# Kernel optimization log

Measured on AMD Instinct MI355X. Metric: run time of the kernel, lower is better.

## Reference

```python
import jax, jax.numpy as jnp
import numpy as np

EMBED_DIM = 1024
NUM_HEADS = 16
HEAD_DIM = EMBED_DIM // NUM_HEADS


def setup_inputs() -> dict:
    key = jax.random.key(0)
    ks = jax.random.split(key, 10)
    s = 1.0 / np.sqrt(EMBED_DIM)
    x = jax.random.normal(ks[0], (2, 2048, EMBED_DIM), dtype=jnp.float32)
    Wq = jax.random.uniform(ks[1], (EMBED_DIM, EMBED_DIM), jnp.float32, -s, s)
    bq = jax.random.uniform(ks[2], (EMBED_DIM,), jnp.float32, -s, s)
    Wk = jax.random.uniform(ks[3], (EMBED_DIM, EMBED_DIM), jnp.float32, -s, s)
    bk = jax.random.uniform(ks[4], (EMBED_DIM,), jnp.float32, -s, s)
    Wv = jax.random.uniform(ks[5], (EMBED_DIM, EMBED_DIM), jnp.float32, -s, s)
    bv = jax.random.uniform(ks[6], (EMBED_DIM,), jnp.float32, -s, s)
    Wo = jax.random.uniform(ks[7], (EMBED_DIM, EMBED_DIM), jnp.float32, -s, s)
    bo = jax.random.uniform(ks[8], (EMBED_DIM,), jnp.float32, -s, s)
    return {"x": x, "Wq": Wq, "bq": bq, "Wk": Wk, "bk": bk,
            "Wv": Wv, "bv": bv, "Wo": Wo, "bo": bo}


def reference(x, Wq, bq, Wk, bk, Wv, bv, Wo, bo):
    b, s, e = x.shape
    h, d = NUM_HEADS, HEAD_DIM
    scale = d ** -0.5
    # projections (torch Linear: x @ W.T + b; here W stored as [in, out])
    q = (x @ Wq + bq).reshape(b, s, h, d)
    k = (x @ Wk + bk).reshape(b, s, h, d)
    v = (x @ Wv + bv).reshape(b, s, h, d)
    logits = jnp.einsum('bqhd,bkhd->bhqk', q, k) * scale
    causal = jnp.tril(jnp.ones((s, s), dtype=bool))  # keep lower triangle
    logits = jnp.where(causal, logits, -jnp.inf)
    attn = jax.nn.softmax(logits, axis=-1)
    out = jnp.einsum('bhqk,bkhd->bqhd', attn, v).reshape(b, s, e)
    return out @ Wo + bo
```

## Files before the change

kernel.cpp:

```cpp
#include <hip/hip_runtime.h>


#define EMB 1024
#define SEQ 2048
#define NB 2
#define NH 16
#define HD 64

#define QSCALE 0.18033688011112042f

typedef float f32x4 __attribute__((ext_vector_type(4)));
typedef float floatx4 __attribute__((ext_vector_type(4)));
typedef short short8 __attribute__((ext_vector_type(8)));
typedef __bf16 bf16x8 __attribute__((ext_vector_type(8)));
typedef __bf16 bf16x2 __attribute__((ext_vector_type(2)));
typedef unsigned short ushortx4 __attribute__((ext_vector_type(4)));
typedef unsigned int uintx4 __attribute__((ext_vector_type(4)));

__device__ __forceinline__ unsigned short bf16u(float f) {
  __bf16 h = (__bf16)f;
  return __builtin_bit_cast(unsigned short, h);
}

__device__ __forceinline__ unsigned pkbf(float lo, float hi) {
  bf16x2 v;
  v[0] = (__bf16)lo;
  v[1] = (__bf16)hi;
  return __builtin_bit_cast(unsigned, v);
}

__device__ __forceinline__ f32x4 mfma16(short8 a, short8 b, f32x4 c) {
  return __builtin_amdgcn_mfma_f32_16x16x32_bf16(
      __builtin_bit_cast(bf16x8, a), __builtin_bit_cast(bf16x8, b), c, 0, 0, 0);
}

__device__ __forceinline__ void gload16(const void* g, void* lds) {
  __builtin_amdgcn_global_load_lds(
      (const __attribute__((address_space(1))) unsigned int*)g,
      (__attribute__((address_space(3))) unsigned int*)lds, 16, 0, 0);
}

__global__ __launch_bounds__(256) void cvt_x_kernel(
    const float* __restrict__ x, unsigned short* __restrict__ out) {
  const int idx = (blockIdx.x * 256 + threadIdx.x) * 4;
  floatx4 v = *(const floatx4*)(x + idx);
  ushortx4 o;
  #pragma unroll
  for (int i = 0; i < 4; ++i) o[i] = bf16u(v[i]);
  *(ushortx4*)(out + idx) = o;
}

__global__ __launch_bounds__(256) void cvt_w4_kernel(
    const float* __restrict__ W0, const float* __restrict__ W1,
    const float* __restrict__ W2, const float* __restrict__ W3,
    unsigned short* __restrict__ T0, unsigned short* __restrict__ T1,
    unsigned short* __restrict__ T2, unsigned short* __restrict__ T3) {
  __shared__ unsigned short tile[32][33];
  const int z = blockIdx.z;
  const float* W = (z == 0) ? W0 : (z == 1) ? W1 : (z == 2) ? W2 : W3;
  unsigned short* WT = (z == 0) ? T0 : (z == 1) ? T1 : (z == 2) ? T2 : T3;
  const int k0 = blockIdx.x * 32, n0 = blockIdx.y * 32;
  const int t = threadIdx.x;
  const int r = t >> 3, c = (t & 7) * 4;
  floatx4 v = *(const floatx4*)(W + (k0 + r) * EMB + n0 + c);
  #pragma unroll
  for (int i = 0; i < 4; ++i) tile[r][c + i] = bf16u(v[i]);
  __syncthreads();
  ushortx4 o;
  #pragma unroll
  for (int i = 0; i < 4; ++i) o[i] = tile[c + i][r];
  *(ushortx4*)(WT + (n0 + r) * EMB + k0 + c) = o;
}

#define GEMM_KLOOP(OP1, OP2)                                                 \
    for (int kk = 0; kk < 64; kk += 32) {                                    \
      short8 a[4], b[4];                                                     \
      _Pragma("unroll")                                                      \
      for (int i = 0; i < 4; ++i)                                            \
        a[i] = *(const short8*)(As + (wr * 64 + i * 16 + ln) * 64 + kk + g * 8); \
      _Pragma("unroll")                                                      \
      for (int j = 0; j < 4; ++j)                                            \
        b[j] = *(const short8*)(Bs + (wc * 64 + j * 16 + ln) * 64 + kk + g * 8); \
      _Pragma("unroll")                                                      \
      for (int i = 0; i < 4; ++i)                                            \
        _Pragma("unroll")                                                    \
        for (int j = 0; j < 4; ++j)                                          \
          acc[i][j] = mfma16(OP1, OP2, acc[i][j]);                           \
    }

__global__ __launch_bounds__(256) void gemm_qkv_kernel(
    const unsigned short* __restrict__ Xb,
    const unsigned short* __restrict__ W0, const unsigned short* __restrict__ W1,
    const unsigned short* __restrict__ W2,
    const float* __restrict__ b0, const float* __restrict__ b1,
    const float* __restrict__ b2,
    unsigned short* __restrict__ Qo, unsigned short* __restrict__ Ko,
    unsigned short* __restrict__ Vo) {
  __shared__ __align__(16) unsigned short As[128 * 64];
  __shared__ __align__(16) unsigned short Bs[128 * 64];
  const int z = blockIdx.z;
  const unsigned short* Wt = (z == 0) ? W0 : ((z == 1) ? W1 : W2);
  const float* bias = (z == 0) ? b0 : ((z == 1) ? b1 : b2);
  const bool sw = (z != 2);
  const int m0 = blockIdx.y * 128, n0 = blockIdx.x * 128;
  const int tid = threadIdx.x, l = tid & 63, w = tid >> 6;
  const int g = l >> 4, ln = l & 15;
  const int wr = w >> 1, wc = w & 1;

  f32x4 acc[4][4];
  #pragma unroll
  for (int i = 0; i < 4; ++i)
    #pragma unroll
    for (int j = 0; j < 4; ++j) acc[i][j] = (f32x4){0.f, 0.f, 0.f, 0.f};

  for (int kt = 0; kt < 16; ++kt) {
    const int kb = kt * 64;
    #pragma unroll
    for (int it = 0; it < 4; ++it) {
      const int chunk = w * 4 + it;
      const int lin = chunk * 64 + l;
      const int row = lin >> 3, col = (lin & 7) * 8;
      gload16(Xb + (m0 + row) * EMB + kb + col, (char*)As + chunk * 1024);
      gload16(Wt + (n0 + row) * EMB + kb + col, (char*)Bs + chunk * 1024);
    }
    __syncthreads();
    if (sw) {
      GEMM_KLOOP(b[j], a[i])
    } else {
      GEMM_KLOOP(a[i], b[j])
    }
    __syncthreads();
  }

  const int mb = m0 + wr * 64, nb = n0 + wc * 64;
  if (sw) {
    unsigned short* dst = (z == 0) ? Qo : Ko;
    const float osc = (z == 0) ? QSCALE : 1.0f;
    #pragma unroll
    for (int j = 0; j < 4; ++j) {
      const int n = nb + j * 16 + 4 * g;
      floatx4 bv_ = *(const floatx4*)(bias + n);
      const int h = n >> 6, d = n & 63;
      #pragma unroll
      for (int i = 0; i < 4; ++i) {
        const int m = mb + i * 16 + ln;
        const int bb = m >> 11, ss = m & 2047;
        ushortx4 o;
        #pragma unroll
        for (int e = 0; e < 4; ++e) o[e] = bf16u((acc[i][j][e] + bv_[e]) * osc);
        *(ushortx4*)(dst + ((bb * NH + h) * SEQ + ss) * HD + d) = o;
      }
    }
  } else {
    #pragma unroll
    for (int j = 0; j < 4; ++j) {
      const int n = nb + j * 16 + ln;
      const float bgain = bias[n];
      const int h = n >> 6, d = n & 63;
      #pragma unroll
      for (int i = 0; i < 4; ++i) {
        const int mf = mb + i * 16 + 4 * g;
        const int bb = mf >> 11, ss = mf & 2047;
        ushortx4 o;
        #pragma unroll
        for (int e = 0; e < 4; ++e) o[e] = bf16u(acc[i][j][e] + bgain);
        *(ushortx4*)(Vo + ((bb * NH + h) * HD + d) * SEQ + ss) = o;
      }
    }
  }
}

__global__ __launch_bounds__(512) void attn_kernel(
    const unsigned short* __restrict__ Q, const unsigned short* __restrict__ K,
    const unsigned short* __restrict__ Vt, unsigned short* __restrict__ O) {
  __shared__ __align__(16) unsigned short Kt[2][64 * 64];
  __shared__ __align__(16) unsigned short Vl[2][64 * 64];
  const int id = blockIdx.x;
  const int bh = id & 31;
  const int T = 15 - (id >> 5);
  const int h = bh & 15, b = bh >> 4;
  const int tid = threadIdx.x, l = tid & 63, w = tid >> 6;
  const int g = l >> 4, ln = l & 15;
  const size_t baseQK = (size_t)bh * SEQ * HD;
  const size_t baseV = (size_t)bh * HD * SEQ;
  const int xr = ln & 7;
  const int srcA = ((g & 1) << 5) + ln;
  const int srcB = srcA + 16;
  const bool hi = (g >> 1) != 0;

  const int st_row = w * 8 + (l >> 3);
  const int csw = (l & 7) ^ ((l >> 3) & 7);

  const int nkt = 2 * T + 2;
  const int qw = T * 128 + w * 16;

  gload16(K + baseQK + (size_t)st_row * HD + csw * 8,
          (char*)&Kt[0][0] + w * 1024);
  gload16(Vt + baseV + (size_t)st_row * SEQ + csw * 8,
          (char*)&Vl[0][0] + w * 1024);

  const int qrow = qw + ln;
  short8 qf0 = *(const short8*)(Q + baseQK + (size_t)qrow * HD + g * 8);
  short8 qf1 = *(const short8*)(Q + baseQK + (size_t)qrow * HD + 32 + g * 8);

  float m_run = -1e30f, l_run = 0.f;
  f32x4 acc[4];
  #pragma unroll
  for (int dj = 0; dj < 4; ++dj) acc[dj] = (f32x4){0.f, 0.f, 0.f, 0.f};

  #pragma unroll 1
  for (int kt = 0; kt < nkt; ++kt) {
    const int cur = kt & 1;
    const bool has_next = (kt + 1 < nkt);
    if (has_next) {
      const int nxt = cur ^ 1;
      const int kn = kt + 1;
      gload16(K + baseQK + (size_t)(kn * 64 + st_row) * HD + csw * 8,
              (char*)&Kt[nxt][0] + w * 1024);
      gload16(Vt + baseV + (size_t)st_row * SEQ + kn * 64 + csw * 8,
              (char*)&Vl[nxt][0] + w * 1024);
      asm volatile("s_waitcnt vmcnt(2)" ::: "memory");
    } else {
      asm volatile("s_waitcnt vmcnt(0)" ::: "memory");
    }
    __builtin_amdgcn_s_barrier();

    const int deff = 8 * T + w - 4 * kt;
    if (deff >= 0) {
      const int jmax = (deff > 3) ? 3 : deff;

      f32x4 sv[4];
      #pragma unroll
      for (int j = 0; j < 4; ++j)
        sv[j] = (f32x4){-1e30f, -1e30f, -1e30f, -1e30f};
      __builtin_amdgcn_s_setprio(1);
      #pragma unroll
      for (int j = 0; j < 4; ++j) {
        if (j <= jmax) {
          f32x4 t = (f32x4){0.f, 0.f, 0.f, 0.f};
          short8 kf0 = *(const short8*)(
              &Kt[cur][(j * 16 + ln) * 64 + ((g ^ xr) * 8)]);
          t = mfma16(kf0, qf0, t);
          short8 kf1 = *(const short8*)(
              &Kt[cur][(j * 16 + ln) * 64 + (((4 + g) ^ xr) * 8)]);
          t = mfma16(kf1, qf1, t);
          if (j == deff) {
            #pragma unroll
            for (int e = 0; e < 4; ++e)
              sv[j][e] = (4 * g + e <= ln) ? t[e] : -1e30f;
          } else {
            sv[j] = t;
          }
        }
      }
      __builtin_amdgcn_s_setprio(0);

      float tj[4];
      #pragma unroll
      for (int j = 0; j < 4; ++j)
        tj[j] = fmaxf(fmaxf(sv[j][0], sv[j][1]), fmaxf(sv[j][2], sv[j][3]));
      float tm = fmaxf(fmaxf(tj[0], tj[1]), fmaxf(tj[2], tj[3]));
      tm = fmaxf(tm, __shfl_xor(tm, 16));
      tm = fmaxf(tm, __shfl_xor(tm, 32));
      const float nm = fmaxf(m_run, tm);
      const float al = exp2f(m_run - nm);
      m_run = nm;

      float p[4][4];
      float rs = 0.f;
      #pragma unroll
      for (int j = 0; j < 4; ++j)
        #pragma unroll
        for (int e = 0; e < 4; ++e) {
          p[j][e] = exp2f(sv[j][e] - nm);
          rs += p[j][e];
        }
      rs += __shfl_xor(rs, 16);
      rs += __shfl_xor(rs, 32);
      l_run = l_run * al + rs;
      #pragma unroll
      for (int dj = 0; dj < 4; ++dj) acc[dj] *= al;

      unsigned pk[4][2];
      #pragma unroll
      for (int j = 0; j < 4; ++j) {
        pk[j][0] = pkbf(p[j][0], p[j][1]);
        pk[j][1] = pkbf(p[j][2], p[j][3]);
      }

      const int ksmax = (jmax >= 2) ? 2 : 1;
      short8 pf0, pf1;
      {
        unsigned a0 = __shfl(pk[0][0], srcA), a1 = __shfl(pk[0][1], srcA);
        unsigned a2 = __shfl(pk[0][0], srcB), a3 = __shfl(pk[0][1], srcB);
        unsigned b0 = __shfl(pk[1][0], srcA), b1 = __shfl(pk[1][1], srcA);
        unsigned b2 = __shfl(pk[1][0], srcB), b3 = __shfl(pk[1][1], srcB);
        uintx4 u;
        u[0] = hi ? b0 : a0; u[1] = hi ? b1 : a1;
        u[2] = hi ? b2 : a2; u[3] = hi ? b3 : a3;
        pf0 = __builtin_bit_cast(short8, u);
      }
      if (ksmax > 1) {
        unsigned a0 = __shfl(pk[2][0], srcA), a1 = __shfl(pk[2][1], srcA);
        unsigned a2 = __shfl(pk[2][0], srcB), a3 = __shfl(pk[2][1], srcB);
        unsigned b0 = __shfl(pk[3][0], srcA), b1 = __shfl(pk[3][1], srcA);
        unsigned b2 = __shfl(pk[3][0], srcB), b3 = __shfl(pk[3][1], srcB);
        uintx4 u;
        u[0] = hi ? b0 : a0; u[1] = hi ? b1 : a1;
        u[2] = hi ? b2 : a2; u[3] = hi ? b3 : a3;
        pf1 = __builtin_bit_cast(short8, u);
      }

      __builtin_amdgcn_s_setprio(1);
      #pragma unroll
      for (int dj = 0; dj < 4; ++dj) {
        short8 vb0 = *(const short8*)(
            &Vl[cur][(dj * 16 + ln) * 64 + ((g ^ xr) * 8)]);
        acc[dj] = mfma16(vb0, pf0, acc[dj]);
        if (ksmax > 1) {
          short8 vb1 = *(const short8*)(
              &Vl[cur][(dj * 16 + ln) * 64 + (((4 + g) ^ xr) * 8)]);
          acc[dj] = mfma16(vb1, pf1, acc[dj]);
        }
      }
      __builtin_amdgcn_s_setprio(0);
    }

    asm volatile("" ::: "memory");
    __builtin_amdgcn_s_barrier();
  }

  const float inv = 1.f / l_run;
  const size_t orow = ((size_t)b * SEQ + qw + ln) * EMB + h * HD;
  #pragma unroll
  for (int dj = 0; dj < 4; ++dj) {
    ushortx4 o;
    #pragma unroll
    for (int e = 0; e < 4; ++e) o[e] = bf16u(acc[dj][e] * inv);
    *(ushortx4*)(O + orow + dj * 16 + 4 * g) = o;
  }
}

__global__ __launch_bounds__(256) void gemm_o_kernel(
    const unsigned short* __restrict__ Ab, const unsigned short* __restrict__ Wt,
    const float* __restrict__ bias, float* __restrict__ out) {
  __shared__ __align__(16) unsigned short As[128 * 64];
  __shared__ __align__(16) unsigned short Bs[128 * 64];
  const int m0 = blockIdx.y * 128, n0 = blockIdx.x * 128;
  const int tid = threadIdx.x, l = tid & 63, w = tid >> 6;
  const int g = l >> 4, ln = l & 15;
  const int wr = w >> 1, wc = w & 1;

  f32x4 acc[4][4];
  #pragma unroll
  for (int i = 0; i < 4; ++i)
    #pragma unroll
    for (int j = 0; j < 4; ++j) acc[i][j] = (f32x4){0.f, 0.f, 0.f, 0.f};

  for (int kt = 0; kt < 16; ++kt) {
    const int kb = kt * 64;
    #pragma unroll
    for (int it = 0; it < 4; ++it) {
      const int chunk = w * 4 + it;
      const int lin = chunk * 64 + l;
      const int row = lin >> 3, col = (lin & 7) * 8;
      gload16(Ab + (m0 + row) * EMB + kb + col, (char*)As + chunk * 1024);
      gload16(Wt + (n0 + row) * EMB + kb + col, (char*)Bs + chunk * 1024);
    }
    __syncthreads();
    GEMM_KLOOP(b[j], a[i])
    __syncthreads();
  }

  const int mb = m0 + wr * 64, nb = n0 + wc * 64;
  #pragma unroll
  for (int j = 0; j < 4; ++j) {
    const int n = nb + j * 16 + 4 * g;
    floatx4 bv_ = *(const floatx4*)(bias + n);
    #pragma unroll
    for (int i = 0; i < 4; ++i) {
      const int m = mb + i * 16 + ln;
      floatx4 o = acc[i][j] + bv_;
      *(floatx4*)(out + (size_t)m * EMB + n) = o;
    }
  }
}

extern "C" void kernel_launch(void* const* d_in, const int* in_sizes, int n_in,
                              void* d_out, int out_size, void* d_ws, size_t ws_size,
                              hipStream_t stream) {
  const float* x  = (const float*)d_in[0];
  const float* Wq = (const float*)d_in[1];
  const float* bq = (const float*)d_in[2];
  const float* Wk = (const float*)d_in[3];
  const float* bk = (const float*)d_in[4];
  const float* Wv = (const float*)d_in[5];
  const float* bv = (const float*)d_in[6];
  const float* Wo = (const float*)d_in[7];
  const float* bo = (const float*)d_in[8];
  float* out = (float*)d_out;

  char* ws = (char*)d_ws;
  unsigned short* Xb  = (unsigned short*)(ws);
  unsigned short* WqT = (unsigned short*)(ws + 8388608);
  unsigned short* WkT = (unsigned short*)(ws + 10485760);
  unsigned short* WvT = (unsigned short*)(ws + 12582912);
  unsigned short* WoT = (unsigned short*)(ws + 14680064);
  unsigned short* Qb  = (unsigned short*)(ws + 16777216);
  unsigned short* Kb  = (unsigned short*)(ws + 25165824);
  unsigned short* Vtb = (unsigned short*)(ws + 33554432);
  unsigned short* Ao  = Xb;

  hipLaunchKernelGGL(cvt_x_kernel, dim3(4096), dim3(256), 0, stream, x, Xb);
  hipLaunchKernelGGL(cvt_w4_kernel, dim3(32, 32, 4), dim3(256), 0, stream,
                     Wq, Wk, Wv, Wo, WqT, WkT, WvT, WoT);
  hipLaunchKernelGGL(gemm_qkv_kernel, dim3(8, 32, 3), dim3(256), 0, stream,
                     Xb, WqT, WkT, WvT, bq, bk, bv, Qb, Kb, Vtb);
  hipLaunchKernelGGL(attn_kernel, dim3(512), dim3(512), 0, stream,
                     Qb, Kb, Vtb, Ao);
  hipLaunchKernelGGL(gemm_o_kernel, dim3(8, 32), dim3(256), 0, stream,
                     Ao, WoT, bo, out);
}
```

Baseline: 168.4 us.

## Double attention key tile to 128 keys per iteration

The attention kernel now processes 128 keys per loop iteration instead of 64, which halves the iteration count and the number of block barriers and online-softmax rescales. Each wave computes 8 score fragments and up to 4 PV k-steps per iteration, and the V tile gets a new 16-wide XOR swizzle. Shared memory doubles to 64 KB and register pressure grows from the larger score and P arrays, which may reduce occupancy. Causal skipping also becomes coarser, so more masked work is done on the diagonal tile.

```diff
diff --git a/kernel.cpp b/kernel.cpp
--- a/kernel.cpp
+++ b/kernel.cpp
@@ -173,8 +173,8 @@
 __global__ __launch_bounds__(512) void attn_kernel(
     const unsigned short* __restrict__ Q, const unsigned short* __restrict__ K,
     const unsigned short* __restrict__ Vt, unsigned short* __restrict__ O) {
-  __shared__ __align__(16) unsigned short Kt[2][64 * 64];
-  __shared__ __align__(16) unsigned short Vl[2][64 * 64];
+  __shared__ __align__(16) unsigned short Kt[2][128 * 64];
+  __shared__ __align__(16) unsigned short Vl[2][64 * 128];
   const int id = blockIdx.x;
   const int bh = id & 31;
   const int T = 15 - (id >> 5);
@@ -188,16 +188,22 @@
   const int srcB = srcA + 16;
   const bool hi = (g >> 1) != 0;
 
-  const int st_row = w * 8 + (l >> 3);
-  const int csw = (l & 7) ^ ((l >> 3) & 7);
-
-  const int nkt = 2 * T + 2;
+  const int kr0 = (2 * w) * 8 + (l >> 3), kr1 = (2 * w + 1) * 8 + (l >> 3);
+  const int kc0 = (l & 7) ^ (kr0 & 7), kc1 = (l & 7) ^ (kr1 & 7);
+  const int vr0 = (2 * w) * 4 + (l >> 4), vr1 = (2 * w + 1) * 4 + (l >> 4);
+  const int vc0 = (l & 15) ^ (vr0 & 15), vc1 = (l & 15) ^ (vr1 & 15);
+
+  const int nkt = T + 1;
   const int qw = T * 128 + w * 16;
 
-  gload16(K + baseQK + (size_t)st_row * HD + csw * 8,
-          (char*)&Kt[0][0] + w * 1024);
-  gload16(Vt + baseV + (size_t)st_row * SEQ + csw * 8,
-          (char*)&Vl[0][0] + w * 1024);
+  gload16(K + baseQK + (size_t)kr0 * HD + kc0 * 8,
+          (char*)&Kt[0][0] + (2 * w) * 1024);
+  gload16(K + baseQK + (size_t)kr1 * HD + kc1 * 8,
+          (char*)&Kt[0][0] + (2 * w + 1) * 1024);
+  gload16(Vt + baseV + (size_t)vr0 * SEQ + vc0 * 8,
+          (char*)&Vl[0][0] + (2 * w) * 1024);
+  gload16(Vt + baseV + (size_t)vr1 * SEQ + vc1 * 8,
+          (char*)&Vl[0][0] + (2 * w + 1) * 1024);
 
   const int qrow = qw + ln;
   short8 qf0 = *(const short8*)(Q + baseQK + (size_t)qrow * HD + g * 8);
@@ -214,117 +220,111 @@
     const bool has_next = (kt + 1 < nkt);
     if (has_next) {
       const int nxt = cur ^ 1;
-      const int kn = kt + 1;
-      gload16(K + baseQK + (size_t)(kn * 64 + st_row) * HD + csw * 8,
-              (char*)&Kt[nxt][0] + w * 1024);
-      gload16(Vt + baseV + (size_t)st_row * SEQ + kn * 64 + csw * 8,
-              (char*)&Vl[nxt][0] + w * 1024);
-      asm volatile("s_waitcnt vmcnt(2)" ::: "memory");
+      const size_t kof = (size_t)(kt + 1) * 128;
+      gload16(K + baseQK + (kof + kr0) * HD + kc0 * 8,
+              (char*)&Kt[nxt][0] + (2 * w) * 1024);
+      gload16(K + baseQK + (kof + kr1) * HD + kc1 * 8,
+              (char*)&Kt[nxt][0] + (2 * w + 1) * 1024);
+      gload16(Vt + baseV + (size_t)vr0 * SEQ + kof + vc0 * 8,
+              (char*)&Vl[nxt][0] + (2 * w) * 1024);
+      gload16(Vt + baseV + (size_t)vr1 * SEQ + kof + vc1 * 8,
+              (char*)&Vl[nxt][0] + (2 * w + 1) * 1024);
+      asm volatile("s_waitcnt vmcnt(4)" ::: "memory");
     } else {
       asm volatile("s_waitcnt vmcnt(0)" ::: "memory");
     }
     __builtin_amdgcn_s_barrier();
 
-    const int deff = 8 * T + w - 4 * kt;
-    if (deff >= 0) {
-      const int jmax = (deff > 3) ? 3 : deff;
-
-      f32x4 sv[4];
-      #pragma unroll
-      for (int j = 0; j < 4; ++j)
-        sv[j] = (f32x4){-1e30f, -1e30f, -1e30f, -1e30f};
-      __builtin_amdgcn_s_setprio(1);
-      #pragma unroll
-      for (int j = 0; j < 4; ++j) {
-        if (j <= jmax) {
-          f32x4 t = (f32x4){0.f, 0.f, 0.f, 0.f};
-          short8 kf0 = *(const short8*)(
-              &Kt[cur][(j * 16 + ln) * 64 + ((g ^ xr) * 8)]);
-          t = mfma16(kf0, qf0, t);
-          short8 kf1 = *(const short8*)(
-              &Kt[cur][(j * 16 + ln) * 64 + (((4 + g) ^ xr) * 8)]);
-          t = mfma16(kf1, qf1, t);
-          if (j == deff) {
-            #pragma unroll
-            for (int e = 0; e < 4; ++e)
-              sv[j][e] = (4 * g + e <= ln) ? t[e] : -1e30f;
-          } else {
-            sv[j] = t;
-          }
+    const bool last = (kt == T);
+    const int jmax = last ? w : 7;
+
+    f32x4 sv[8];
+    #pragma unroll
+    for (int j = 0; j < 8; ++j)
+      sv[j] = (f32x4){-1e30f, -1e30f, -1e30f, -1e30f};
+    __builtin_amdgcn_s_setprio(1);
+    #pragma unroll
+    for (int j = 0; j < 8; ++j) {
+      if (j <= jmax) {
+        f32x4 t = (f32x4){0.f, 0.f, 0.f, 0.f};
+        short8 kf0 = *(const short8*)(
+            &Kt[cur][(j * 16 + ln) * 64 + ((g ^ xr) * 8)]);
+        t = mfma16(kf0, qf0, t);
+        short8 kf1 = *(const short8*)(
+            &Kt[cur][(j * 16 + ln) * 64 + (((4 + g) ^ xr) * 8)]);
+        t = mfma16(kf1, qf1, t);
+        if (last && j == w) {
+          #pragma unroll
+          for (int e = 0; e < 4; ++e)
+            sv[j][e] = (4 * g + e <= ln) ? t[e] : -1e30f;
+        } else {
+          sv[j] = t;
         }
       }
-      __builtin_amdgcn_s_setprio(0);
-
-      float tj[4];
-      #pragma unroll
-      for (int j = 0; j < 4; ++j)
-        tj[j] = fmaxf(fmaxf(sv[j][0], sv[j][1]), fmaxf(sv[j][2], sv[j][3]));
-      float tm = fmaxf(fmaxf(tj[0], tj[1]), fmaxf(tj[2], tj[3]));
-      tm = fmaxf(tm, __shfl_xor(tm, 16));
-      tm = fmaxf(tm, __shfl_xor(tm, 32));
-      const float nm = fmaxf(m_run, tm);
-      const float al = exp2f(m_run - nm);
-      m_run = nm;
-
-      float p[4][4];
-      float rs = 0.f;
-      #pragma unroll
-      for (int j = 0; j < 4; ++j)
-        #pragma unroll
-        for (int e = 0; e < 4; ++e) {
-          p[j][e] = exp2f(sv[j][e] - nm);
-          rs += p[j][e];
-        }
-      rs += __shfl_xor(rs, 16);
-      rs += __shfl_xor(rs, 32);
-      l_run = l_run * al + rs;
-      #pragma unroll
-      for (int dj = 0; dj < 4; ++dj) acc[dj] *= al;
-
-      unsigned pk[4][2];
-      #pragma unroll
-      for (int j = 0; j < 4; ++j) {
-        pk[j][0] = pkbf(p[j][0], p[j][1]);
-        pk[j][1] = pkbf(p[j][2], p[j][3]);
-      }
-
-      const int ksmax = (jmax >= 2) ? 2 : 1;
-      short8 pf0, pf1;
-      {
-        unsigned a0 = __shfl(pk[0][0], srcA), a1 = __shfl(pk[0][1], srcA);
-        unsigned a2 = __shfl(pk[0][0], srcB), a3 = __shfl(pk[0][1], srcB);
-        unsigned b0 = __shfl(pk[1][0], srcA), b1 = __shfl(pk[1][1], srcA);
-        unsigned b2 = __shfl(pk[1][0], srcB), b3 = __shfl(pk[1][1], srcB);
+    }
+    __builtin_amdgcn_s_setprio(0);
+
+    float tj[8];
+    #pragma unroll
+    for (int j = 0; j < 8; ++j)
+      tj[j] = fmaxf(fmaxf(sv[j][0], sv[j][1]), fmaxf(sv[j][2], sv[j][3]));
+    float tm = fmaxf(fmaxf(fmaxf(tj[0], tj[1]), fmaxf(tj[2], tj[3])),
+                     fmaxf(fmaxf(tj[4], tj[5]), fmaxf(tj[6], tj[7])));
+    tm = fmaxf(tm, __shfl_xor(tm, 16));
+    tm = fmaxf(tm, __shfl_xor(tm, 32));
+    const float nm = fmaxf(m_run, tm);
+    const float al = exp2f(m_run - nm);
+    m_run = nm;
+
+    unsigned pk[8][2];
+    float rs = 0.f;
+    #pragma unroll
+    for (int j = 0; j < 8; ++j) {
+      const float p0 = exp2f(sv[j][0] - nm), p1 = exp2f(sv[j][1] - nm);
+      const float p2 = exp2f(sv[j][2] - nm), p3 = exp2f(sv[j][3] - nm);
+      rs += (p0 + p1) + (p2 + p3);
+      pk[j][0] = pkbf(p0, p1);
+      pk[j][1] = pkbf(p2, p3);
+    }
+    rs += __shfl_xor(rs, 16);
+    rs += __shfl_xor(rs, 32);
+    l_run = l_run * al + rs;
+    #pragma unroll
+    for (int dj = 0; dj < 4; ++dj) acc[dj] *= al;
+
+    const int ksmax = (jmax >> 1) + 1;
+    short8 pf[4];
+    #pragma unroll
+    for (int ks = 0; ks < 4; ++ks) {
+      if (ks < ksmax) {
+        unsigned a0 = __shfl(pk[2 * ks][0], srcA);
+        unsigned a1 = __shfl(pk[2 * ks][1], srcA);
+        unsigned a2 = __shfl(pk[2 * ks][0], srcB);
+        unsigned a3 = __shfl(pk[2 * ks][1], srcB);
+        unsigned b0 = __shfl(pk[2 * ks + 1][0], srcA);
+        unsigned b1 = __shfl(pk[2 * ks + 1][1], srcA);
+        unsigned b2 = __shfl(pk[2 * ks + 1][0], srcB);
+        unsigned b3 = __shfl(pk[2 * ks + 1][1], srcB);
         uintx4 u;
         u[0] = hi ? b0 : a0; u[1] = hi ? b1 : a1;
         u[2] = hi ? b2 : a2; u[3] = hi ? b3 : a3;
-        pf0 = __builtin_bit_cast(short8, u);
+        pf[ks] = __builtin_bit_cast(short8, u);
       }
-      if (ksmax > 1) {
-        unsigned a0 = __shfl(pk[2][0], srcA), a1 = __shfl(pk[2][1], srcA);
-        unsigned a2 = __shfl(pk[2][0], srcB), a3 = __shfl(pk[2][1], srcB);
-        unsigned b0 = __shfl(pk[3][0], srcA), b1 = __shfl(pk[3][1], srcA);
-        unsigned b2 = __shfl(pk[3][0], srcB), b3 = __shfl(pk[3][1], srcB);
-        uintx4 u;
-        u[0] = hi ? b0 : a0; u[1] = hi ? b1 : a1;
-        u[2] = hi ? b2 : a2; u[3] = hi ? b3 : a3;
-        pf1 = __builtin_bit_cast(short8, u);
-      }
-
-      __builtin_amdgcn_s_setprio(1);
+    }
+
+    __builtin_amdgcn_s_setprio(1);
+    #pragma unroll
+    for (int dj = 0; dj < 4; ++dj) {
       #pragma unroll
-      for (int dj = 0; dj < 4; ++dj) {
-        short8 vb0 = *(const short8*)(
-            &Vl[cur][(dj * 16 + ln) * 64 + ((g ^ xr) * 8)]);
-        acc[dj] = mfma16(vb0, pf0, acc[dj]);
-        if (ksmax > 1) {
-          short8 vb1 = *(const short8*)(
-              &Vl[cur][(dj * 16 + ln) * 64 + (((4 + g) ^ xr) * 8)]);
-          acc[dj] = mfma16(vb1, pf1, acc[dj]);
+      for (int ks = 0; ks < 4; ++ks) {
+        if (ks < ksmax) {
+          short8 vb = *(const short8*)(
+              &Vl[cur][(dj * 16 + ln) * 128 + (((ks * 4 + g) ^ ln) * 8)]);
+          acc[dj] = mfma16(vb, pf[ks], acc[dj]);
         }
       }
-      __builtin_amdgcn_s_setprio(0);
-    }
+    }
+    __builtin_amdgcn_s_setprio(0);
 
     asm volatile("" ::: "memory");
     __builtin_amdgcn_s_barrier();
```

Measured after the change: 164.6 us. 1.02x faster.
